# Optimization experiments

Hardware: AMD Instinct MI355X
Metric: run time of the kernel (lower is better)

Reference implementation:

```python
import jax, jax.numpy as jnp
import numpy as np

ALPHA = 0.05
KSIZE = 7
SIGMA = 7.0  # SecondMomentMatrixLayer calls get_gaussian_kernel(ksize, ksize)


def _gaussian_kernel(ksize, sigma):
    ax = np.arange(ksize, dtype=np.float32) - (ksize - 1) / 2.0
    g1 = np.exp(-(ax ** 2) / (2.0 * sigma ** 2))
    g2 = np.outer(g1, g1)
    g2 = g2 / g2.sum()
    return jnp.asarray(g2, dtype=jnp.float32)


def setup_inputs() -> dict:
    key = jax.random.key(0)
    x = jax.random.uniform(key, (1, 1, 2048, 4096), dtype=jnp.float32)
    # Sobel filters (cross-correlation weights, as torch conv2d uses)
    wx = jnp.array([[-1., 0., 1.], [-2., 0., 2.], [-1., 0., 1.]], dtype=jnp.float32)
    wy = wx.T
    sobel_w = jnp.stack([wx, wy], axis=0)[:, None]  # (2,1,3,3)
    gauss_w = _gaussian_kernel(KSIZE, SIGMA)[None, None]  # (1,1,7,7)
    return {"x": x, "sobel_w": sobel_w, "gauss_w": gauss_w}


def _conv_same(x, w, groups=1):
    # x: (N,C,H,W), w: (O,C/g,kh,kw); torch-style cross-correlation, SAME padding
    return jax.lax.conv_general_dilated(
        x, w, window_strides=(1, 1), padding="SAME",
        dimension_numbers=("NCHW", "OIHW", "NCHW"),
        feature_group_count=groups)


def reference(x, sobel_w, gauss_w):
    # 1) image gradients: (N,1,H,W) -> (N,2,H,W)
    g = _conv_same(x, sobel_w)
    ix, iy = g[:, 0], g[:, 1]  # (N,H,W)
    # 2) channel products Ixx, Iyy, Ixy: (N,3,H,W)
    prod = jnp.stack([ix * ix, iy * iy, ix * iy], axis=1)
    # 3) Gaussian smoothing of each channel (same kernel depthwise)
    gw3 = jnp.broadcast_to(gauss_w, (3, 1, KSIZE, KSIZE))
    s = _conv_same(prod, gw3, groups=3)
    sxx, syy, sxy = s[:, 0], s[:, 1], s[:, 2]  # (N,H,W)
    # 4) corner response R = det - alpha*trace^2 (with the original's extra unsqueeze(0))
    r = (sxx * syy - sxy * sxy) - ALPHA * ((sxx + syy) ** 2)[None]  # (1,N,H,W) -> (1,1,H,W) for N=1
    # 5) NMS: threshold at (lower) median, 7x7 stride-1 maxpool, equality mask, multiply
    flat = r.ravel()
    k = (flat.shape[0] - 1) // 2  # torch.median -> lower median
    med = jnp.partition(flat, k)[k]
    thr = jnp.where(r > med, r, jnp.float32(0))
    pooled = jax.lax.reduce_window(
        thr, -jnp.inf, jax.lax.max, (1, 1, KSIZE, KSIZE), (1, 1, 1, 1), "SAME")
    mask = jnp.where(pooled == thr, jnp.float32(1), jnp.float32(0))
    return mask * r
```

## Files before the change

### kernel.cpp

```cpp
#include <hip/hip_runtime.h>
#include <hip/hip_bf16.h>
#include <math.h>

#define H 2048
#define W 4096
#define NPIX (H * W)
#define KSEL 4194303u
#define NT 512
#define TSX 64
#define TSY 32
#define NBX (W / TSX)
#define NBY (H / TSY)

__device__ __forceinline__ unsigned fmap(float f) {
    unsigned u = __float_as_uint(f);
    return (u & 0x80000000u) ? ~u : (u | 0x80000000u);
}
__device__ __forceinline__ float4 ld4s(const float* p) { return *(const float4*)p; }
__device__ __forceinline__ void st4s(float* p, float4 v) { *(float4*)p = v; }
__device__ __forceinline__ void ld12(const float* p, float* d) {
    float4 a = ld4s(p), b = ld4s(p + 4), c = ld4s(p + 8);
    d[0]=a.x; d[1]=a.y; d[2]=a.z; d[3]=a.w;
    d[4]=b.x; d[5]=b.y; d[6]=b.z; d[7]=b.w;
    d[8]=c.x; d[9]=c.y; d[10]=c.z; d[11]=c.w;
}

#define SMF 13480
#define SXA(r,c) smem[5472 + (r)*76 + (c)]
#define GXA(r,c) smem[(r)*72 + (c)]
#define GYA(r,c) smem[2736 + (r)*72 + (c)]
#define H0A(r,c) smem[5472 + (r)*68 + (c)]
#define H1A(r,c) smem[8056 + (r)*68 + (c)]
#define H2A(r,c) smem[10640 + (r)*68 + (c)]

__global__ __launch_bounds__(NT) void k_response(const float* __restrict__ x,
                                                 const float* __restrict__ gw,
                                                 float* __restrict__ r,
                                                 unsigned* __restrict__ hist1) {
    __shared__ float smem[SMF];
    unsigned* lh = (unsigned*)&smem[13224];

    int tl = threadIdx.x;
    int bx = blockIdx.x & (NBX - 1);
    int by = blockIdx.x >> 6;
    int tx0 = bx * TSX, ty0 = by * TSY;
    bool interior = ((unsigned)(bx - 1) < 62u) && ((unsigned)(by - 1) < 62u);

    float hwr[7], vwr[7];
    float g33 = gw[24];
#pragma unroll
    for (int b = 0; b < 7; ++b) hwr[b] = gw[21 + b];
#pragma unroll
    for (int a = 0; a < 7; ++a) vwr[a] = gw[a * 7 + 3] / g33;

    if (tl < 256) lh[tl] = 0;

#pragma unroll
    for (int it = 0; it < 2; ++it) {
        int task = tl + it * NT;
        if (task < 720) {
            int row = task / 18, g = task - row * 18;
            int gy = ty0 - 4 + row;
            int gx0 = tx0 - 4 + 4 * g;
            float4 v;
            if (interior) {
                v = *(const float4*)&x[(size_t)gy * W + gx0];
            } else {
                v = make_float4(0.f, 0.f, 0.f, 0.f);
                if ((unsigned)gy < H) {
                    if ((unsigned)gx0 <= (unsigned)(W - 4)) {
                        v = *(const float4*)&x[(size_t)gy * W + gx0];
                    } else {
                        float* vv = (float*)&v;
#pragma unroll
                        for (int k = 0; k < 4; ++k) {
                            int c = gx0 + k;
                            if ((unsigned)c < W) vv[k] = x[(size_t)gy * W + c];
                        }
                    }
                }
            }
            st4s(&SXA(row, 4 * g), v);
        }
    }
    __syncthreads();

#pragma unroll
    for (int it = 0; it < 2; ++it) {
        int task = tl + it * NT;
        if (task < 684) {
            int row = task / 18, g = task - row * 18;
            int base = 4 * g;
            float w0[8], w1[8], w2[8];
            {
                float4 t0 = ld4s(&SXA(row, base)), t1 = ld4s(&SXA(row, base + 4));
                w0[0]=t0.x; w0[1]=t0.y; w0[2]=t0.z; w0[3]=t0.w; w0[4]=t1.x; w0[5]=t1.y; w0[6]=t1.z; w0[7]=t1.w;
                t0 = ld4s(&SXA(row + 1, base)); t1 = ld4s(&SXA(row + 1, base + 4));
                w1[0]=t0.x; w1[1]=t0.y; w1[2]=t0.z; w1[3]=t0.w; w1[4]=t1.x; w1[5]=t1.y; w1[6]=t1.z; w1[7]=t1.w;
                t0 = ld4s(&SXA(row + 2, base)); t1 = ld4s(&SXA(row + 2, base + 4));
                w2[0]=t0.x; w2[1]=t0.y; w2[2]=t0.z; w2[3]=t0.w; w2[4]=t1.x; w2[5]=t1.y; w2[6]=t1.z; w2[7]=t1.w;
            }
            float4 gxv, gyv;
            float* pgx = (float*)&gxv;
            float* pgy = (float*)&gyv;
            if (interior) {
#pragma unroll
                for (int k = 0; k < 4; ++k) {
                    pgx[k] = (w0[k + 2] - w0[k]) + 2.f * (w1[k + 2] - w1[k]) + (w2[k + 2] - w2[k]);
                    pgy[k] = (w2[k] - w0[k]) + 2.f * (w2[k + 1] - w0[k + 1]) + (w2[k + 2] - w0[k + 2]);
                }
            } else {
                int rowOK = ((unsigned)(ty0 - 3 + row) < H);
#pragma unroll
                for (int k = 0; k < 4; ++k) {
                    float ixv = (w0[k + 2] - w0[k]) + 2.f * (w1[k + 2] - w1[k]) + (w2[k + 2] - w2[k]);
                    float iyv = (w2[k] - w0[k]) + 2.f * (w2[k + 1] - w0[k + 1]) + (w2[k + 2] - w0[k + 2]);
                    int gc = tx0 + base + k - 3;
                    bool ok = rowOK && ((unsigned)gc < W);
                    pgx[k] = ok ? ixv : 0.f;
                    pgy[k] = ok ? iyv : 0.f;
                }
            }
            st4s(&GXA(row, base), gxv);
            st4s(&GYA(row, base), gyv);
        }
    }
    __syncthreads();

#pragma unroll
    for (int it = 0; it < 2; ++it) {
        int task = tl + it * NT;
        if (task < 608) {
            int row = task >> 4, c0 = (task & 15) * 4;
            float wgx[12], wgy[12];
            ld12(&GXA(row, c0), wgx);
            ld12(&GYA(row, c0), wgy);
            float px[10], py[10], pxy[10];
#pragma unroll
            for (int i = 0; i < 10; ++i) {
                px[i] = wgx[i] * wgx[i];
                py[i] = wgy[i] * wgy[i];
                pxy[i] = wgx[i] * wgy[i];
            }
            float4 s0, s1, s2;
            float* q0 = (float*)&s0; float* q1 = (float*)&s1; float* q2 = (float*)&s2;
#pragma unroll
            for (int k = 0; k < 4; ++k) {
                float a0 = 0.f, a1 = 0.f, a2 = 0.f;
#pragma unroll
                for (int b = 0; b < 7; ++b) {
                    float w = hwr[b];
                    a0 += w * px[k + b];
                    a1 += w * py[k + b];
                    a2 += w * pxy[k + b];
                }
                q0[k] = a0; q1[k] = a1; q2[k] = a2;
            }
            st4s(&H0A(row, c0), s0);
            st4s(&H1A(row, c0), s1);
            st4s(&H2A(row, c0), s2);
        }
    }
    __syncthreads();

    {
        int ii = tl >> 4, c0 = (tl & 15) * 4;
        float4 a0 = make_float4(0.f, 0.f, 0.f, 0.f), a1 = a0, a2 = a0;
#pragma unroll
        for (int a = 0; a < 7; ++a) {
            float w = vwr[a];
            float4 h0v = ld4s(&H0A(ii + a, c0));
            float4 h1v = ld4s(&H1A(ii + a, c0));
            float4 h2v = ld4s(&H2A(ii + a, c0));
            a0.x += w * h0v.x; a0.y += w * h0v.y; a0.z += w * h0v.z; a0.w += w * h0v.w;
            a1.x += w * h1v.x; a1.y += w * h1v.y; a1.z += w * h1v.z; a1.w += w * h1v.w;
            a2.x += w * h2v.x; a2.y += w * h2v.y; a2.z += w * h2v.z; a2.w += w * h2v.w;
        }
        float* sxx = (float*)&a0; float* syy = (float*)&a1; float* sxy = (float*)&a2;
        float4 rv4;
        float* prv = (float*)&rv4;
#pragma unroll
        for (int k = 0; k < 4; ++k) {
            float tr = sxx[k] + syy[k];
            prv[k] = sxx[k] * syy[k] - sxy[k] * sxy[k] - 0.05f * tr * tr;
        }
        st4s(&r[(size_t)(ty0 + ii) * W + tx0 + c0], rv4);
#pragma unroll
        for (int k = 0; k < 4; ++k) atomicAdd(&lh[fmap(prv[k]) >> 24], 1u);
    }
    __syncthreads();
    if (tl < 256 && lh[tl]) atomicAdd(&hist1[tl], lh[tl]);
}

__global__ __launch_bounds__(256) void k_scan256(const unsigned* __restrict__ hist,
                                                 unsigned* __restrict__ sel,
                                                 int in_rank_idx, int out_base) {
    __shared__ unsigned s[256];
    int t = threadIdx.x;
    unsigned c = hist[t];
    s[t] = c;
    __syncthreads();
    for (int off = 1; off < 256; off <<= 1) {
        unsigned v = (t >= off) ? s[t - off] : 0u;
        __syncthreads();
        s[t] += v;
        __syncthreads();
    }
    unsigned k = (in_rank_idx < 0) ? KSEL : sel[in_rank_idx];
    unsigned cumb = s[t] - c;
    if (k >= cumb && k < s[t]) {
        sel[out_base] = (unsigned)t;
        sel[out_base + 1] = k - cumb;
    }
}

__global__ __launch_bounds__(256) void k_hist2(const float* __restrict__ r,
                                               const unsigned* __restrict__ sel,
                                               unsigned* __restrict__ hist2) {
    __shared__ unsigned lh[256];
    lh[threadIdx.x] = 0;
    __syncthreads();
    unsigned b1 = sel[0];
    int idx = blockIdx.x * blockDim.x + threadIdx.x;
    int stride = gridDim.x * blockDim.x;
    const float4* r4 = (const float4*)r;
    for (int i = idx; i < NPIX / 4; i += stride) {
        float4 v = r4[i];
        unsigned u;
        u = fmap(v.x); if ((u >> 24) == b1) atomicAdd(&lh[(u >> 16) & 0xFF], 1u);
        u = fmap(v.y); if ((u >> 24) == b1) atomicAdd(&lh[(u >> 16) & 0xFF], 1u);
        u = fmap(v.z); if ((u >> 24) == b1) atomicAdd(&lh[(u >> 16) & 0xFF], 1u);
        u = fmap(v.w); if ((u >> 24) == b1) atomicAdd(&lh[(u >> 16) & 0xFF], 1u);
    }
    __syncthreads();
    if (lh[threadIdx.x]) atomicAdd(&hist2[threadIdx.x], lh[threadIdx.x]);
}

__global__ __launch_bounds__(256) void k_hist3(const float* __restrict__ r,
                                               const unsigned* __restrict__ sel,
                                               unsigned* __restrict__ hist3) {
    unsigned top16 = (sel[0] << 8) | sel[2];
    int idx = blockIdx.x * blockDim.x + threadIdx.x;
    int stride = gridDim.x * blockDim.x;
    const float4* r4 = (const float4*)r;
    for (int i = idx; i < NPIX / 4; i += stride) {
        float4 v = r4[i];
        unsigned u;
        u = fmap(v.x); if ((u >> 16) == top16) atomicAdd(&hist3[u & 0xFFFF], 1u);
        u = fmap(v.y); if ((u >> 16) == top16) atomicAdd(&hist3[u & 0xFFFF], 1u);
        u = fmap(v.z); if ((u >> 16) == top16) atomicAdd(&hist3[u & 0xFFFF], 1u);
        u = fmap(v.w); if ((u >> 16) == top16) atomicAdd(&hist3[u & 0xFFFF], 1u);
    }
}

__global__ __launch_bounds__(1024) void k_scan64k(const unsigned* __restrict__ hist3,
                                                  unsigned* __restrict__ sel) {
    __shared__ unsigned ps[1024];
    int t = threadIdx.x;
    const uint4* h4 = (const uint4*)hist3;
    unsigned sum = 0;
#pragma unroll
    for (int i = 0; i < 16; ++i) {
        uint4 v = h4[t * 16 + i];
        sum += v.x + v.y + v.z + v.w;
    }
    ps[t] = sum;
    __syncthreads();
    for (int off = 1; off < 1024; off <<= 1) {
        unsigned v = (t >= off) ? ps[t - off] : 0u;
        __syncthreads();
        ps[t] += v;
        __syncthreads();
    }
    unsigned k = sel[3];
    unsigned inc = ps[t], cumb = inc - sum;
    if (k >= cumb && k < inc) {
        unsigned rem = k - cumb;
        unsigned cum = 0, b3 = 0;
        for (int i = 0; i < 64; ++i) {
            unsigned c = hist3[t * 64 + i];
            if (rem < cum + c) { b3 = (unsigned)(t * 64 + i); break; }
            cum += c;
        }
        unsigned med_u = (sel[0] << 24) | (sel[2] << 16) | b3;
        unsigned bits = (med_u & 0x80000000u) ? (med_u & 0x7FFFFFFFu) : ~med_u;
        ((float*)sel)[6] = __uint_as_float(bits);
    }
}

#define RT(r,c) smem[(r)*72 + (c)]
#define HM(r,c) smem[2736 + (r)*64 + (c)]

__global__ __launch_bounds__(NT) void k_final(const float* __restrict__ r,
                                              const unsigned* __restrict__ sel,
                                              float* __restrict__ out) {
    __shared__ float smem[5168];
    float med = ((const float*)sel)[6];
    int tl = threadIdx.x;
    int bx = blockIdx.x & (NBX - 1);
    int by = blockIdx.x >> 6;
    int tx0 = bx * TSX, ty0 = by * TSY;
    bool interior = ((unsigned)(bx - 1) < 62u) && ((unsigned)(by - 1) < 62u);
    const float NINF = -INFINITY;

#pragma unroll
    for (int it = 0; it < 2; ++it) {
        int task = tl + it * NT;
        if (task < 684) {
            int row = task / 18, g = task - row * 18;
            int gy = ty0 - 3 + row;
            int gx0 = tx0 - 4 + 4 * g;
            float4 v;
            if (interior) {
                v = *(const float4*)&r[(size_t)gy * W + gx0];
            } else {
                v = make_float4(NINF, NINF, NINF, NINF);
                if ((unsigned)gy < H) {
                    if ((unsigned)gx0 <= (unsigned)(W - 4)) {
                        v = *(const float4*)&r[(size_t)gy * W + gx0];
                    } else {
                        float* pv = (float*)&v;
#pragma unroll
                        for (int k = 0; k < 4; ++k) {
                            int c = gx0 + k;
                            if ((unsigned)c < W) pv[k] = r[(size_t)gy * W + c];
                        }
                    }
                }
            }
            st4s(&RT(row, 4 * g), v);
        }
    }
    __syncthreads();

#pragma unroll
    for (int it = 0; it < 2; ++it) {
        int task = tl + it * NT;
        if (task < 608) {
            int row = task >> 4, c0 = (task & 15) << 2;
            float w[12];
            ld12(&RT(row, c0), w);
            float th[11];
#pragma unroll
            for (int j = 1; j <= 10; ++j) {
                float v = w[j];
                th[j] = (v > med) ? v : ((v == NINF) ? NINF : 0.f);
            }
            float4 m4;
            float* pm = (float*)&m4;
#pragma unroll
            for (int k = 0; k < 4; ++k) {
                float m = th[k + 1];
#pragma unroll
                for (int b = 2; b < 8; ++b) m = fmaxf(m, th[k + b]);
                pm[k] = m;
            }
            st4s(&HM(row, c0), m4);
        }
    }
    __syncthreads();

    {
        int ii = tl >> 4, c0 = (tl & 15) << 2;
        float4 m = ld4s(&HM(ii, c0));
#pragma unroll
        for (int a = 1; a < 7; ++a) {
            float4 h = ld4s(&HM(ii + a, c0));
            m.x = fmaxf(m.x, h.x); m.y = fmaxf(m.y, h.y);
            m.z = fmaxf(m.z, h.z); m.w = fmaxf(m.w, h.w);
        }
        float4 rv = ld4s(&RT(ii + 3, c0 + 4));
        float4 o;
        float tvx = (rv.x > med) ? rv.x : 0.f;
        float tvy = (rv.y > med) ? rv.y : 0.f;
        float tvz = (rv.z > med) ? rv.z : 0.f;
        float tvw = (rv.w > med) ? rv.w : 0.f;
        o.x = (m.x == tvx) ? rv.x : 0.f;
        o.y = (m.y == tvy) ? rv.y : 0.f;
        o.z = (m.z == tvz) ? rv.z : 0.f;
        o.w = (m.w == tvw) ? rv.w : 0.f;
        st4s(&out[(size_t)(ty0 + ii) * W + tx0 + c0], o);
    }
}

extern "C" void kernel_launch(void* const* d_in, const int* in_sizes, int n_in,
                              void* d_out, int out_size, void* d_ws, size_t ws_size,
                              hipStream_t stream) {
    const float* x = (const float*)d_in[0];
    const float* gw = (const float*)d_in[2];
    float* out = (float*)d_out;

    char* ws = (char*)d_ws;
    float* r = (float*)ws;
    unsigned* hist1 = (unsigned*)(ws + (size_t)NPIX * 4);
    unsigned* hist2 = hist1 + 256;
    unsigned* hist3 = hist2 + 256;
    unsigned* sel = hist3 + 65536;

    hipMemsetAsync(hist1, 0, (256 + 256 + 65536 + 8) * sizeof(unsigned), stream);

    int nblk = NBX * NBY;
    k_response<<<nblk, NT, 0, stream>>>(x, gw, r, hist1);
    k_scan256<<<1, 256, 0, stream>>>(hist1, sel, -1, 0);
    k_hist2<<<1024, 256, 0, stream>>>(r, sel, hist2);
    k_scan256<<<1, 256, 0, stream>>>(hist2, sel, 1, 2);
    k_hist3<<<1024, 256, 0, stream>>>(r, sel, hist3);
    k_scan64k<<<1, 1024, 0, stream>>>(hist3, sel);
    k_final<<<nblk, NT, 0, stream>>>(r, sel, out);
}
```

Before: 142.6 us.

## Fuse second histogram scan into hist2 via last-block ticket; shrink LDS

Removes the separate single-block k_scan256 launch after k_hist2. The last block to finish k_hist2, identified by an atomic ticket counter, now does the prefix scan and bucket selection. The local histogram in k_response now reuses the start of shared memory after the tile data is consumed, which lowers the LDS footprint and may improve occupancy at the cost of an extra barrier. The workspace layout and memset grow to include the ticket counter.

```diff
diff --git a/kernel.cpp b/kernel.cpp
--- a/kernel.cpp
+++ b/kernel.cpp
@@ -24,8 +24,11 @@
     d[4]=b.x; d[5]=b.y; d[6]=b.z; d[7]=b.w;
     d[8]=c.x; d[9]=c.y; d[10]=c.z; d[11]=c.w;
 }
-
-#define SMF 13480
+__device__ __forceinline__ unsigned aload(const unsigned* p) {
+    return __hip_atomic_load(p, __ATOMIC_RELAXED, __HIP_MEMORY_SCOPE_AGENT);
+}
+
+#define SMF 13224
 #define SXA(r,c) smem[5472 + (r)*76 + (c)]
 #define GXA(r,c) smem[(r)*72 + (c)]
 #define GYA(r,c) smem[2736 + (r)*72 + (c)]
@@ -38,7 +41,7 @@
                                                  float* __restrict__ r,
                                                  unsigned* __restrict__ hist1) {
     __shared__ float smem[SMF];
-    unsigned* lh = (unsigned*)&smem[13224];
+    unsigned* lh = (unsigned*)smem;
 
     int tl = threadIdx.x;
     int bx = blockIdx.x & (NBX - 1);
@@ -52,8 +55,6 @@
     for (int b = 0; b < 7; ++b) hwr[b] = gw[21 + b];
 #pragma unroll
     for (int a = 0; a < 7; ++a) vwr[a] = gw[a * 7 + 3] / g33;
-
-    if (tl < 256) lh[tl] = 0;
 
 #pragma unroll
     for (int it = 0; it < 2; ++it) {
@@ -163,6 +164,9 @@
     }
     __syncthreads();
 
+    if (tl < 256) lh[tl] = 0;
+    __syncthreads();
+
     {
         int ii = tl >> 4, c0 = (tl & 15) * 4;
         float4 a0 = make_float4(0.f, 0.f, 0.f, 0.f), a1 = a0, a2 = a0;
@@ -215,13 +219,16 @@
 }
 
 __global__ __launch_bounds__(256) void k_hist2(const float* __restrict__ r,
-                                               const unsigned* __restrict__ sel,
-                                               unsigned* __restrict__ hist2) {
+                                               unsigned* __restrict__ sel,
+                                               unsigned* __restrict__ hist2,
+                                               unsigned* __restrict__ tick) {
     __shared__ unsigned lh[256];
-    lh[threadIdx.x] = 0;
+    __shared__ unsigned lastf;
+    int t = threadIdx.x;
+    lh[t] = 0;
     __syncthreads();
     unsigned b1 = sel[0];
-    int idx = blockIdx.x * blockDim.x + threadIdx.x;
+    int idx = blockIdx.x * blockDim.x + t;
     int stride = gridDim.x * blockDim.x;
     const float4* r4 = (const float4*)r;
     for (int i = idx; i < NPIX / 4; i += stride) {
@@ -233,7 +240,27 @@
         u = fmap(v.w); if ((u >> 24) == b1) atomicAdd(&lh[(u >> 16) & 0xFF], 1u);
     }
     __syncthreads();
-    if (lh[threadIdx.x]) atomicAdd(&hist2[threadIdx.x], lh[threadIdx.x]);
+    if (lh[t]) atomicAdd(&hist2[t], lh[t]);
+    __syncthreads();
+
+    if (t == 0)
+        lastf = (__hip_atomic_fetch_add(tick, 1u, __ATOMIC_ACQ_REL, __HIP_MEMORY_SCOPE_AGENT)
+                 == (unsigned)(gridDim.x - 1)) ? 1u : 0u;
+    __syncthreads();
+    if (lastf) {
+        unsigned c = aload(&hist2[t]);
+        lh[t] = c;
+        __syncthreads();
+        for (int off = 1; off < 256; off <<= 1) {
+            unsigned v = (t >= off) ? lh[t - off] : 0u;
+            __syncthreads();
+            lh[t] += v;
+            __syncthreads();
+        }
+        unsigned k = sel[1];
+        unsigned cumb = lh[t] - c;
+        if (k >= cumb && k < lh[t]) { sel[2] = (unsigned)t; sel[3] = k - cumb; }
+    }
 }
 
 __global__ __launch_bounds__(256) void k_hist3(const float* __restrict__ r,
@@ -392,18 +419,19 @@
 
     char* ws = (char*)d_ws;
     float* r = (float*)ws;
-    unsigned* hist1 = (unsigned*)(ws + (size_t)NPIX * 4);
-    unsigned* hist2 = hist1 + 256;
-    unsigned* hist3 = hist2 + 256;
-    unsigned* sel = hist3 + 65536;
-
-    hipMemsetAsync(hist1, 0, (256 + 256 + 65536 + 8) * sizeof(unsigned), stream);
+    unsigned* base = (unsigned*)(ws + (size_t)NPIX * 4);
+    unsigned* hist1 = base;
+    unsigned* hist2 = base + 256;
+    unsigned* hist3 = base + 512;
+    unsigned* sel   = base + 66048;
+    unsigned* tick  = base + 66064;
+
+    hipMemsetAsync(base, 0, 66068u * sizeof(unsigned), stream);
 
     int nblk = NBX * NBY;
     k_response<<<nblk, NT, 0, stream>>>(x, gw, r, hist1);
     k_scan256<<<1, 256, 0, stream>>>(hist1, sel, -1, 0);
-    k_hist2<<<1024, 256, 0, stream>>>(r, sel, hist2);
-    k_scan256<<<1, 256, 0, stream>>>(hist2, sel, 1, 2);
+    k_hist2<<<1024, 256, 0, stream>>>(r, sel, hist2, tick);
     k_hist3<<<1024, 256, 0, stream>>>(r, sel, hist3);
     k_scan64k<<<1, 1024, 0, stream>>>(hist3, sel);
     k_final<<<nblk, NT, 0, stream>>>(r, sel, out);
```

New measurement: 146.9 us. 3.0% more time.
